# Performance work log

Measured on AMD Instinct MI355X. Metric: run time of the kernel, lower is better.

The kernel has to match this reference:

```python
import jax, jax.numpy as jnp
import numpy as np

N_NODES = 50000
N_EDGES = 400000
N_GRAPHS = 256
HID = 128
FEAT_IN, POS_IN, EDGE_IN = 64, 16, 16
N_LAYERS = 4


def _lin(x, w, b):
    return x @ w.T + b


def setup_inputs() -> dict:
    key = jax.random.key(0)
    ks = iter(jax.random.split(key, 64))
    s = 0.05

    def w(shape):
        return (jax.random.normal(next(ks), shape, dtype=jnp.float32) * s)

    inp = {
        "h": jax.random.normal(next(ks), (N_NODES, FEAT_IN), dtype=jnp.float32),
        "e": jax.random.normal(next(ks), (N_EDGES, EDGE_IN), dtype=jnp.float32),
        "p": jax.random.normal(next(ks), (N_NODES, POS_IN), dtype=jnp.float32),
        "edge_index": jax.random.randint(next(ks), (2, N_EDGES), 0, N_NODES),
        "batch": jnp.sort(jax.random.randint(next(ks), (N_NODES,), 0, N_GRAPHS)),
        # embeddings
        "h_embed_w": w((HID, FEAT_IN)), "h_embed_b": w((HID,)),
        "e_embed_w": w((HID, EDGE_IN)), "e_embed_b": w((HID,)),
        "p_embed_w": w((HID, POS_IN)), "p_embed_b": w((HID,)),
        # per-layer params, stacked over layers
        "hu_w": w((N_LAYERS, HID, 5 * HID)), "hu_b": w((N_LAYERS, HID)),
        "eu_w": w((N_LAYERS, HID, 3 * HID)), "eu_b": w((N_LAYERS, HID)),
        "pu_w": w((N_LAYERS, HID, 3 * HID)), "pu_b": w((N_LAYERS, HID)),
        "hagg_w": w((N_LAYERS, HID, 2 * HID)), "hagg_b": w((N_LAYERS, HID)),
        "pagg_w": w((N_LAYERS, HID, 2 * HID)), "pagg_b": w((N_LAYERS, HID)),
        # readout MLP
        "r1_w": w((HID, 2 * HID)), "r1_b": w((HID,)),
        "r2_w": w((HID // 2, HID)), "r2_b": w((HID // 2,)),
        "r3_w": w((1, HID // 2)), "r3_b": w((1,)),
    }
    return inp


def reference(h, e, p, edge_index, batch,
              h_embed_w, h_embed_b, e_embed_w, e_embed_b, p_embed_w, p_embed_b,
              hu_w, hu_b, eu_w, eu_b, pu_w, pu_b,
              hagg_w, hagg_b, pagg_w, pagg_b,
              r1_w, r1_b, r2_w, r2_b, r3_w, r3_b):
    send, rec = edge_index[0], edge_index[1]
    N = h.shape[0]

    h = _lin(h, h_embed_w, h_embed_b)
    e = _lin(e, e_embed_w, e_embed_b)
    p = _lin(p, p_embed_w, p_embed_b)

    for l in range(N_LAYERS):
        hp_send = jnp.concatenate((h[send], p[send]), axis=1)  # [E, 2H]
        hp_rec = jnp.concatenate((h[rec], p[rec]), axis=1)     # [E, 2H]
        h_msg = _lin(jnp.concatenate((hp_send, hp_rec, e), axis=1), hu_w[l], hu_b[l])
        h_msg_agg = jax.ops.segment_sum(h_msg, rec, num_segments=N)
        h = _lin(jnp.concatenate((h, h_msg_agg), axis=1), hagg_w[l], hagg_b[l])
        e = _lin(jnp.concatenate((h[send], h[rec], e), axis=1), eu_w[l], eu_b[l])
        p_msg = _lin(jnp.concatenate((p[send], p[rec], e), axis=1), pu_w[l], pu_b[l])
        p_msg_agg = jax.ops.segment_sum(p_msg, rec, num_segments=N)
        p = _lin(jnp.concatenate((p, p_msg_agg), axis=1), pagg_w[l], pagg_b[l])

    h_agg = jax.ops.segment_sum(h, batch, num_segments=N_GRAPHS)
    p_agg = jax.ops.segment_sum(p, batch, num_segments=N_GRAPHS)
    hep = jnp.concatenate((h_agg, p_agg), axis=1)
    x = jax.nn.relu(_lin(hep, r1_w, r1_b))
    x = jax.nn.relu(_lin(x, r2_w, r2_b))
    out = _lin(x, r3_w, r3_b).squeeze(-1)  # [N_GRAPHS]
    return (out, p)
```

## Files before the change

kernel.cpp:

```cpp
#include <hip/hip_runtime.h>

typedef __attribute__((ext_vector_type(8))) short bf16x8;
typedef __attribute__((ext_vector_type(4))) float f32x4;
typedef __attribute__((ext_vector_type(4))) unsigned short us4;

__device__ __forceinline__ float b2f(unsigned short h) {
  union { unsigned int u; float f; } v; v.u = ((unsigned int)h) << 16; return v.f;
}
__device__ __forceinline__ unsigned short f2b(float f) {
  union { float f; unsigned int u; } v; v.f = f;
  unsigned int r = v.u + 0x7fffu + ((v.u >> 16) & 1u);
  return (unsigned short)(r >> 16);
}

__global__ void f2b_kernel(const float* __restrict__ in, unsigned short* __restrict__ out, int n4) {
  int i = blockIdx.x * blockDim.x + threadIdx.x;
  int stride = gridDim.x * blockDim.x;
  for (; i < n4; i += stride) {
    float4 v = reinterpret_cast<const float4*>(in)[i];
    us4 o;
    o[0] = f2b(v.x); o[1] = f2b(v.y); o[2] = f2b(v.z); o[3] = f2b(v.w);
    reinterpret_cast<us4*>(out)[i] = o;
  }
}

__launch_bounds__(256)
__global__ void compose_w(const float* __restrict__ hg, const float* __restrict__ hu,
                          const float* __restrict__ pg, const float* __restrict__ pu,
                          const float* __restrict__ hub, const float* __restrict__ pub,
                          unsigned short* __restrict__ wh, unsigned short* __restrict__ wp,
                          float* __restrict__ bh, float* __restrict__ bp) {
  __shared__ float As[128][129];
  __shared__ float Bs[128][36];
  __shared__ float bvs[128];
  const int l = blockIdx.x >> 5, t = blockIdx.x & 31;
  const float* A; const float* B; const float* bv; unsigned short* W; float* bo;
  int lda, ldb, K2, ldw, cbase;
  if (t < 20) {
    A = hg + (size_t)l * 128 * 256; lda = 256;
    B = hu + (size_t)l * 128 * 640; ldb = 640; K2 = 640;
    W = wh + (size_t)l * 128 * 768; ldw = 768;
    bv = hub + l * 128; bo = bh + l * 128; cbase = t * 32;
  } else {
    A = pg + (size_t)l * 128 * 256; lda = 256;
    B = pu + (size_t)l * 128 * 384; ldb = 384; K2 = 384;
    W = wp + (size_t)l * 128 * 512; ldw = 512;
    bv = pub + l * 128; bo = bp + l * 128; cbase = (t - 20) * 32;
  }
  const int tid = threadIdx.x;
  for (int idx = tid; idx < 128 * 128; idx += 256) {
    int r = idx >> 7, c = idx & 127;
    As[r][c] = A[r * lda + 128 + c];
  }
  for (int idx = tid; idx < 128 * 32; idx += 256) {
    int m = idx >> 5, c = idx & 31;
    Bs[m][c] = B[m * ldb + cbase + c];
  }
  if (tid < 128) bvs[tid] = bv[tid];
  __syncthreads();
  const int o = tid & 127, g = tid >> 7;
  float acc[16];
#pragma unroll
  for (int j = 0; j < 16; ++j) acc[j] = 0.f;
  for (int m = 0; m < 128; ++m) {
    float a = As[o][m];
#pragma unroll
    for (int j4 = 0; j4 < 4; ++j4) {
      float4 b4 = *reinterpret_cast<const float4*>(&Bs[m][g * 16 + j4 * 4]);
      acc[j4 * 4 + 0] += a * b4.x; acc[j4 * 4 + 1] += a * b4.y;
      acc[j4 * 4 + 2] += a * b4.z; acc[j4 * 4 + 3] += a * b4.w;
    }
  }
#pragma unroll
  for (int j4 = 0; j4 < 4; ++j4) {
    us4 ov;
    ov[0] = f2b(acc[j4 * 4 + 0]); ov[1] = f2b(acc[j4 * 4 + 1]);
    ov[2] = f2b(acc[j4 * 4 + 2]); ov[3] = f2b(acc[j4 * 4 + 3]);
    *reinterpret_cast<us4*>(&W[(long)o * ldw + cbase + g * 16 + j4 * 4]) = ov;
  }
  if (cbase == 0) {
    for (int idx = tid; idx < 128 * 128; idx += 256) {
      int oo = idx >> 7, m = idx & 127;
      W[(long)oo * ldw + K2 + m] = f2b(A[oo * lda + m]);
    }
    if (tid < 128) {
      float s = 0.f;
      for (int m = 0; m < 128; ++m) s += As[tid][m] * bvs[m];
      bo[tid] = s;
    }
  }
}

template<int K>
__launch_bounds__(256)
__global__ void embed_fast(const float* __restrict__ in, const float* __restrict__ w,
                           const float* __restrict__ b, unsigned short* __restrict__ out,
                           long M, int ostride, int ocoloff, const float* __restrict__ degB,
                           unsigned short* __restrict__ out2, const float* __restrict__ scaleF) {
  __shared__ float wT[K][129];
  __shared__ float xt[16 * K];
  const int tid = threadIdx.x;
  const int col = tid & 127;
  const int half = tid >> 7;
  for (int idx = tid; idx < 128 * K; idx += 256) {
    int c = idx / K, k = idx % K;
    wT[k][c] = w[idx];
  }
  __syncthreads();
  float wreg[K];
#pragma unroll
  for (int k = 0; k < K; ++k) wreg[k] = wT[k][col];
  const float bcol = b[col];

  for (long r0 = (long)blockIdx.x * 16; r0 < M; r0 += (long)gridDim.x * 16) {
    __syncthreads();
    const float4* src4 = reinterpret_cast<const float4*>(in + r0 * K);
    const int n4 = 16 * K / 4;
    if (r0 + 16 <= M) {
      for (int i = tid; i < n4; i += 256)
        reinterpret_cast<float4*>(xt)[i] = src4[i];
    } else {
      int rem = (int)((M - r0) * K) / 4;
      for (int i = tid; i < n4; i += 256) {
        float4 z = {0.f, 0.f, 0.f, 0.f};
        reinterpret_cast<float4*>(xt)[i] = (i < rem) ? src4[i] : z;
      }
    }
    __syncthreads();
#pragma unroll
    for (int rr = 0; rr < 8; ++rr) {
      long row = r0 + half * 8 + rr;
      if (row >= M) break;
      const float* xr = &xt[(half * 8 + rr) * K];
      float acc = bcol * (degB ? degB[row] : 1.0f);
#pragma unroll
      for (int k4 = 0; k4 < K / 4; ++k4) {
        float4 xv = reinterpret_cast<const float4*>(xr)[k4];
        acc += xv.x * wreg[k4 * 4] + xv.y * wreg[k4 * 4 + 1] +
               xv.z * wreg[k4 * 4 + 2] + xv.w * wreg[k4 * 4 + 3];
      }
      long o = row * ostride + ocoloff + col;
      out[o] = f2b(acc);
      if (out2) out2[o] = f2b(acc * scaleF[row]);
    }
  }
}

__global__ void count_deg(const int* __restrict__ rec, int* __restrict__ deg, int E) {
  int i = blockIdx.x * blockDim.x + threadIdx.x;
  if (i < E) atomicAdd(&deg[rec[i]], 1);
}

__global__ void scan_blk(const int* __restrict__ deg, int* __restrict__ tmp,
                         int* __restrict__ blkSum, int N) {
  __shared__ int ts[256];
  const int b = blockIdx.x, t = threadIdx.x;
  const int base = b * 1024 + t * 4;
  int v0 = (base + 0 < N) ? deg[base + 0] : 0;
  int v1 = (base + 1 < N) ? deg[base + 1] : 0;
  int v2 = (base + 2 < N) ? deg[base + 2] : 0;
  int v3 = (base + 3 < N) ? deg[base + 3] : 0;
  int tsum = v0 + v1 + v2 + v3;
  ts[t] = tsum;
  __syncthreads();
  for (int off = 1; off < 256; off <<= 1) {
    int x = (t >= off) ? ts[t - off] : 0;
    __syncthreads();
    ts[t] += x;
    __syncthreads();
  }
  int texcl = ts[t] - tsum;
  if (base + 0 < N) tmp[base + 0] = texcl;
  if (base + 1 < N) tmp[base + 1] = texcl + v0;
  if (base + 2 < N) tmp[base + 2] = texcl + v0 + v1;
  if (base + 3 < N) tmp[base + 3] = texcl + v0 + v1 + v2;
  if (t == 255) blkSum[b] = ts[255];
}

__global__ void scan_top(int* __restrict__ blkSum, int nb) {
  __shared__ int s[64];
  int t = threadIdx.x;
  if (t < nb) s[t] = blkSum[t];
  __syncthreads();
  if (t == 0) {
    int run = 0;
    for (int i = 0; i < nb; ++i) { int x = s[i]; s[i] = run; run += x; }
  }
  __syncthreads();
  if (t < nb) blkSum[t] = s[t];
}

__global__ void scan_fix(const int* __restrict__ deg, int* __restrict__ row_ptr,
                         const int* __restrict__ blkOff, int* __restrict__ cursor,
                         float* __restrict__ degF, int N, int E) {
  const int b = blockIdx.x, t = threadIdx.x;
  const int base = b * 1024 + t * 4;
  const int off = blkOff[b];
#pragma unroll
  for (int k = 0; k < 4; ++k) {
    int i = base + k;
    if (i < N) {
      int v = row_ptr[i] + off;
      row_ptr[i] = v;
      cursor[i] = v;
      degF[i] = (float)deg[i];
    }
  }
  if (b == 0 && t == 0) row_ptr[N] = E;
}

__global__ void scatter_perm(const int* __restrict__ rec, const int* __restrict__ send,
                             int* __restrict__ cursor, int* __restrict__ perm,
                             int* __restrict__ sendP, int E) {
  int i = blockIdx.x * blockDim.x + threadIdx.x;
  if (i < E) {
    int pos = atomicAdd(&cursor[rec[i]], 1);
    perm[pos] = i;
    sendP[pos] = send[i];
  }
}

__global__ void segsum_raw(const float* __restrict__ eraw, const int* __restrict__ row_ptr,
                           const int* __restrict__ perm, float* __restrict__ out16, int N) {
  int sub = threadIdx.x >> 4;
  int f = threadIdx.x & 15;
  int r = blockIdx.x * 16 + sub;
  if (r >= N) return;
  int j0 = row_ptr[r], j1 = row_ptr[r + 1];
  float s0 = 0.f, s1 = 0.f;
  int j = j0;
  for (; j + 2 <= j1; j += 2) {
    int e0 = perm[j], e1 = perm[j + 1];
    s0 += eraw[(long)e0 * 16 + f];
    s1 += eraw[(long)e1 * 16 + f];
  }
  if (j < j1) s0 += eraw[(long)perm[j] * 16 + f];
  out16[(long)r * 16 + f] = s0 + s1;
}

__launch_bounds__(256)
__global__ void gather_sum256(const unsigned short* __restrict__ src,
                              const int* __restrict__ row_ptr, const int* __restrict__ sendP,
                              unsigned short* __restrict__ dst, int N) {
  const int wid = threadIdx.x >> 6, lane = threadIdx.x & 63;
  const int r = blockIdx.x * 4 + wid;
  if (r >= N) return;
  const int j0 = row_ptr[r], j1 = row_ptr[r + 1];
  const int off = lane * 4;
  float a0 = 0.f, a1 = 0.f, a2 = 0.f, a3 = 0.f;
  int j = j0;
  for (; j + 4 <= j1; j += 4) {
    int i0 = sendP[j], i1 = sendP[j + 1], i2 = sendP[j + 2], i3 = sendP[j + 3];
    us4 x = *reinterpret_cast<const us4*>(&src[(long)i0 * 256 + off]);
    us4 y = *reinterpret_cast<const us4*>(&src[(long)i1 * 256 + off]);
    us4 z = *reinterpret_cast<const us4*>(&src[(long)i2 * 256 + off]);
    us4 w = *reinterpret_cast<const us4*>(&src[(long)i3 * 256 + off]);
    a0 += b2f(x[0]) + b2f(y[0]) + b2f(z[0]) + b2f(w[0]);
    a1 += b2f(x[1]) + b2f(y[1]) + b2f(z[1]) + b2f(w[1]);
    a2 += b2f(x[2]) + b2f(y[2]) + b2f(z[2]) + b2f(w[2]);
    a3 += b2f(x[3]) + b2f(y[3]) + b2f(z[3]) + b2f(w[3]);
  }
  for (; j < j1; ++j) {
    us4 x = *reinterpret_cast<const us4*>(&src[(long)sendP[j] * 256 + off]);
    a0 += b2f(x[0]); a1 += b2f(x[1]); a2 += b2f(x[2]); a3 += b2f(x[3]);
  }
  us4 o;
  o[0] = f2b(a0); o[1] = f2b(a1); o[2] = f2b(a2); o[3] = f2b(a3);
  *reinterpret_cast<us4*>(&dst[(long)r * 256 + off]) = o;
}

__launch_bounds__(256)
__global__ void gather_sum128(const unsigned short* __restrict__ src, int col,
                              const int* __restrict__ row_ptr, const int* __restrict__ sendP,
                              unsigned short* __restrict__ dst, int N) {
  const int wid = threadIdx.x >> 6, lane = threadIdx.x & 63;
  const int r = blockIdx.x * 4 + wid;
  if (r >= N) return;
  const int j0 = row_ptr[r], j1 = row_ptr[r + 1];
  const int half = lane >> 5;
  const int c = lane & 31;
  const int off = col + c * 4;
  float a0 = 0.f, a1 = 0.f, a2 = 0.f, a3 = 0.f;
  float b0 = 0.f, b1 = 0.f, b2 = 0.f, b3 = 0.f;
  int j = j0 + half;
  for (; j + 6 < j1; j += 8) {
    int i0 = sendP[j], i1 = sendP[j + 2], i2 = sendP[j + 4], i3 = sendP[j + 6];
    us4 x = *reinterpret_cast<const us4*>(&src[(long)i0 * 256 + off]);
    us4 y = *reinterpret_cast<const us4*>(&src[(long)i1 * 256 + off]);
    us4 z = *reinterpret_cast<const us4*>(&src[(long)i2 * 256 + off]);
    us4 w = *reinterpret_cast<const us4*>(&src[(long)i3 * 256 + off]);
    a0 += b2f(x[0]) + b2f(z[0]); a1 += b2f(x[1]) + b2f(z[1]);
    a2 += b2f(x[2]) + b2f(z[2]); a3 += b2f(x[3]) + b2f(z[3]);
    b0 += b2f(y[0]) + b2f(w[0]); b1 += b2f(y[1]) + b2f(w[1]);
    b2 += b2f(y[2]) + b2f(w[2]); b3 += b2f(y[3]) + b2f(w[3]);
  }
  for (; j + 2 < j1; j += 4) {
    int i0 = sendP[j], i1 = sendP[j + 2];
    us4 x = *reinterpret_cast<const us4*>(&src[(long)i0 * 256 + off]);
    us4 y = *reinterpret_cast<const us4*>(&src[(long)i1 * 256 + off]);
    a0 += b2f(x[0]); a1 += b2f(x[1]); a2 += b2f(x[2]); a3 += b2f(x[3]);
    b0 += b2f(y[0]); b1 += b2f(y[1]); b2 += b2f(y[2]); b3 += b2f(y[3]);
  }
  if (j < j1) {
    us4 x = *reinterpret_cast<const us4*>(&src[(long)sendP[j] * 256 + off]);
    a0 += b2f(x[0]); a1 += b2f(x[1]); a2 += b2f(x[2]); a3 += b2f(x[3]);
  }
  a0 += b0; a1 += b1; a2 += b2; a3 += b3;
  a0 += __shfl_xor(a0, 32); a1 += __shfl_xor(a1, 32);
  a2 += __shfl_xor(a2, 32); a3 += __shfl_xor(a3, 32);
  if (half == 0) {
    us4 o;
    o[0] = f2b(a0); o[1] = f2b(a1); o[2] = f2b(a2); o[3] = f2b(a3);
    *reinterpret_cast<us4*>(&dst[(long)r * 256 + off]) = o;
  }
}

__launch_bounds__(256, 3)
__global__ void gemm_mp(int M, int nsrc, int strides, int coloffs,
                        const unsigned short* __restrict__ sp0, const unsigned short* __restrict__ sp1,
                        const unsigned short* __restrict__ sp2, const unsigned short* __restrict__ sp3,
                        const unsigned short* __restrict__ sp4, const unsigned short* __restrict__ sp5,
                        const unsigned short* __restrict__ Wb,
                        const float* __restrict__ bdeg, const float* __restrict__ bone,
                        const float* __restrict__ degF,
                        unsigned short* __restrict__ outB, int ostride, int ocoloff,
                        unsigned short* __restrict__ outB2, float* __restrict__ outF) {
  __shared__ __align__(16) unsigned short ldsW[8 * 64 * 8];
  const int tid = threadIdx.x;
  const int wid = tid >> 6, lane = tid & 63;
  const int K = nsrc * 128;
  const long rowBase = (long)blockIdx.x * 128 + wid * 32;
  const int lq = lane >> 4;
  const int lr = lane & 15;

  int rowD[2];
#pragma unroll
  for (int am = 0; am < 2; ++am) {
    long e = rowBase + am * 16 + lr;
    if (e >= M) e = M - 1;
    rowD[am] = (int)e;
  }

  f32x4 acc[2][8];
#pragma unroll
  for (int i = 0; i < 2; ++i)
#pragma unroll
    for (int j = 0; j < 8; ++j) acc[i][j] = 0.f;

  for (int si = 0; si < nsrc; ++si) {
    const unsigned short* sp = (si == 0) ? sp0 : (si == 1) ? sp1 : (si == 2) ? sp2
                              : (si == 3) ? sp3 : (si == 4) ? sp4 : sp5;
    const long astride = (long)(((strides >> (si * 4)) & 15) * 128);
    const int acoloff = ((coloffs >> (si * 4)) & 15) * 128;
#pragma unroll
    for (int sub = 0; sub < 4; ++sub) {
      const int koff = acoloff + sub * 32 + lq * 8;
      bf16x8 a[2];
#pragma unroll
      for (int am = 0; am < 2; ++am)
        a[am] = *reinterpret_cast<const bf16x8*>(&sp[(long)rowD[am] * astride + koff]);
      __syncthreads();
#pragma unroll
      for (int it = 0; it < 2; ++it) {
        int idx = tid + it * 256;
        int t = idx >> 6, l = idx & 63;
        int n = t * 16 + (l & 15);
        int kk = si * 128 + sub * 32 + ((l >> 4) * 8);
        *reinterpret_cast<bf16x8*>(&ldsW[idx * 8]) =
            *reinterpret_cast<const bf16x8*>(&Wb[(long)n * K + kk]);
      }
      __syncthreads();
#pragma unroll
      for (int n = 0; n < 8; ++n) {
        bf16x8 b = *reinterpret_cast<const bf16x8*>(&ldsW[(n * 64 + lane) * 8]);
#pragma unroll
        for (int am = 0; am < 2; ++am)
          acc[am][n] = __builtin_amdgcn_mfma_f32_16x16x32_bf16(a[am], b, acc[am][n], 0, 0, 0);
      }
    }
  }

  float bd[8], bo[8];
#pragma unroll
  for (int n = 0; n < 8; ++n) {
    bd[n] = bdeg ? bdeg[n * 16 + lr] : 0.f;
    bo[n] = bone ? bone[n * 16 + lr] : 0.f;
  }

#pragma unroll
  for (int am = 0; am < 2; ++am) {
#pragma unroll
    for (int r = 0; r < 4; ++r) {
      long row = rowBase + am * 16 + lq * 4 + r;
      if (row < M) {
        float d = degF[row];
        long ob = row * ostride + ocoloff;
#pragma unroll
        for (int n = 0; n < 8; ++n) {
          float v = acc[am][n][r] + bd[n] * d + bo[n];
          outB[ob + n * 16 + lr] = f2b(v);
          if (outB2) outB2[ob + n * 16 + lr] = f2b(v * d);
          if (outF) outF[row * 128 + n * 16 + lr] = v;
        }
      }
    }
  }
}

__global__ void readout_agg(const unsigned short* __restrict__ hp,
                            const int* __restrict__ batch, float* __restrict__ hep, int N) {
  int col = threadIdx.x;
  int n0 = blockIdx.x * 128;
  int n1 = n0 + 128; if (n1 > N) n1 = N;
  float sum = 0.f; int curg = -1;
  for (int n = n0; n < n1; ++n) {
    int g = batch[n];
    if (g != curg) {
      if (curg >= 0) unsafeAtomicAdd(&hep[(long)curg * 256 + col], sum);
      curg = g; sum = 0.f;
    }
    sum += b2f(hp[(long)n * 256 + col]);
  }
  if (curg >= 0) unsafeAtomicAdd(&hep[(long)curg * 256 + col], sum);
}

__global__ void mlp_kernel(const float* __restrict__ hep,
                           const float* __restrict__ r1w, const float* __restrict__ r1b,
                           const float* __restrict__ r2w, const float* __restrict__ r2b,
                           const float* __restrict__ r3w, const float* __restrict__ r3b,
                           float* __restrict__ out) {
  int g = blockIdx.x, t = threadIdx.x;
  __shared__ float x[256];
  __shared__ float y[128];
  __shared__ float z[64];
  x[t] = hep[(long)g * 256 + t];
  x[t + 128] = hep[(long)g * 256 + 128 + t];
  __syncthreads();
  float s = r1b[t];
  for (int k = 0; k < 256; ++k) s += r1w[t * 256 + k] * x[k];
  y[t] = fmaxf(s, 0.f);
  __syncthreads();
  if (t < 64) {
    float s2 = r2b[t];
    for (int k = 0; k < 128; ++k) s2 += r2w[t * 128 + k] * y[k];
    z[t] = fmaxf(s2, 0.f);
  }
  __syncthreads();
  if (t == 0) {
    float s3 = r3b[0];
    for (int k = 0; k < 64; ++k) s3 += r3w[k] * z[k];
    out[g] = s3;
  }
}

extern "C" void kernel_launch(void* const* d_in, const int* in_sizes, int n_in,
                              void* d_out, int out_size, void* d_ws, size_t ws_size,
                              hipStream_t stream) {
  const float* h_in = (const float*)d_in[0];
  const float* e_in = (const float*)d_in[1];
  const float* p_in = (const float*)d_in[2];
  const int* ei = (const int*)d_in[3];
  const int* batch = (const int*)d_in[4];
  const float* he_w = (const float*)d_in[5];  const float* he_b = (const float*)d_in[6];
  const float* ee_w = (const float*)d_in[7];  const float* ee_b = (const float*)d_in[8];
  const float* pe_w = (const float*)d_in[9];  const float* pe_b = (const float*)d_in[10];
  const float* hu_w = (const float*)d_in[11]; const float* hu_b = (const float*)d_in[12];
  const float* eu_w = (const float*)d_in[13]; const float* eu_b = (const float*)d_in[14];
  const float* pu_w = (const float*)d_in[15]; const float* pu_b = (const float*)d_in[16];
  const float* hg_w = (const float*)d_in[17]; const float* hg_b = (const float*)d_in[18];
  const float* pg_w = (const float*)d_in[19]; const float* pg_b = (const float*)d_in[20];
  const float* r1w = (const float*)d_in[21];  const float* r1b = (const float*)d_in[22];
  const float* r2w = (const float*)d_in[23];  const float* r2b = (const float*)d_in[24];
  const float* r3w = (const float*)d_in[25];  const float* r3b = (const float*)d_in[26];

  const int N = 50000, E = 400000, G = 256;
  const int* send = ei;
  const int* rec = ei + E;

  char* ws = (char*)d_ws;
  size_t off = 0;
  auto alloc = [&](size_t bytes) {
    void* pp = ws + off;
    off += (bytes + 255) & ~(size_t)255;
    return pp;
  };
  unsigned short* hp  = (unsigned short*)alloc((size_t)N * 256 * 2);
  unsigned short* dhp = (unsigned short*)alloc((size_t)N * 256 * 2);
  unsigned short* gHP = (unsigned short*)alloc((size_t)N * 256 * 2);
  unsigned short* sT  = (unsigned short*)alloc((size_t)N * 128 * 2);
  float* segsumF = (float*)alloc((size_t)N * 16 * 4);
  int* deg = (int*)alloc((size_t)N * 4);
  int* row_ptr = (int*)alloc((size_t)(N + 1) * 4);
  int* cursor = (int*)alloc((size_t)N * 4);
  int* blkSum = (int*)alloc((size_t)64 * 4);
  int* perm = (int*)alloc((size_t)E * 4);
  int* sendP = (int*)alloc((size_t)E * 4);
  float* degF = (float*)alloc((size_t)N * 4);
  float* hep = (float*)alloc((size_t)G * 256 * 4);
  unsigned short* w_h2 = (unsigned short*)alloc((size_t)4 * 128 * 768 * 2);
  unsigned short* w_p2 = (unsigned short*)alloc((size_t)4 * 128 * 512 * 2);
  unsigned short* w_eu = (unsigned short*)alloc((size_t)4 * 128 * 384 * 2);
  float* bh1 = (float*)alloc((size_t)4 * 128 * 4);
  float* bp1 = (float*)alloc((size_t)4 * 128 * 4);
  (void)ws_size; (void)n_in; (void)in_sizes; (void)out_size;

  f2b_kernel<<<192, 256, 0, stream>>>(eu_w, w_eu, 4 * 128 * 384 / 4);
  compose_w<<<128, 256, 0, stream>>>(hg_w, hu_w, pg_w, pu_w, hu_b, pu_b, w_h2, w_p2, bh1, bp1);

  const int nb = (N + 1023) / 1024;
  hipMemsetAsync(deg, 0, (size_t)N * 4, stream);
  count_deg<<<(E + 255) / 256, 256, 0, stream>>>(rec, deg, E);
  scan_blk<<<nb, 256, 0, stream>>>(deg, row_ptr, blkSum, N);
  scan_top<<<1, 64, 0, stream>>>(blkSum, nb);
  scan_fix<<<nb, 256, 0, stream>>>(deg, row_ptr, blkSum, cursor, degF, N, E);
  scatter_perm<<<(E + 255) / 256, 256, 0, stream>>>(rec, send, cursor, perm, sendP, E);

  embed_fast<64><<<3125, 256, 0, stream>>>(h_in, he_w, he_b, hp, N, 256, 0, nullptr, dhp, degF);
  embed_fast<16><<<3125, 256, 0, stream>>>(p_in, pe_w, pe_b, hp, N, 256, 128, nullptr, dhp, degF);
  segsum_raw<<<(N + 15) / 16, 256, 0, stream>>>(e_in, row_ptr, perm, segsumF, N);
  embed_fast<16><<<3125, 256, 0, stream>>>(segsumF, ee_w, ee_b, sT, N, 128, 0, degF, nullptr, nullptr);

  gather_sum256<<<(N + 3) / 4, 256, 0, stream>>>(hp, row_ptr, sendP, gHP, N);

  float* pOut = (float*)d_out + 256;
  const int gridN = (N + 127) / 128;
  const int gridG = (N + 3) / 4;

  for (int l = 0; l < 4; ++l) {
    gemm_mp<<<gridN, 256, 0, stream>>>(N, 6, 0x212222, 0x001010,
        gHP, gHP, dhp, dhp, sT, hp,
        w_h2 + (size_t)l * 128 * 768, bh1 + l * 128, hg_b + l * 128, degF,
        hp, 256, 0, dhp, nullptr);
    gather_sum128<<<gridG, 256, 0, stream>>>(hp, 0, row_ptr, sendP, gHP, N);
    gemm_mp<<<gridN, 256, 0, stream>>>(N, 3, 0x122, 0x000,
        gHP, dhp, sT, nullptr, nullptr, nullptr,
        w_eu + (size_t)l * 128 * 384, eu_b + l * 128, nullptr, degF,
        sT, 128, 0, nullptr, nullptr);
    gemm_mp<<<gridN, 256, 0, stream>>>(N, 4, 0x2122, 0x1011,
        gHP, dhp, sT, hp, nullptr, nullptr,
        w_p2 + (size_t)l * 128 * 512, bp1 + l * 128, pg_b + l * 128, degF,
        hp, 256, 128, (l < 3) ? dhp : nullptr, (l == 3) ? pOut : nullptr);
    if (l < 3)
      gather_sum128<<<gridG, 256, 0, stream>>>(hp, 128, row_ptr, sendP, gHP, N);
  }

  hipMemsetAsync(hep, 0, (size_t)G * 256 * 4, stream);
  readout_agg<<<(N + 127) / 128, 256, 0, stream>>>(hp, batch, hep, N);
  mlp_kernel<<<G, 128, 0, stream>>>(hep, r1w, r1b, r2w, r2b, r3w, r3b, (float*)d_out);
}
```

Before: 700.1 us.

## Drop degree-scaled dhp buffer; scale A fragments by degree inside GEMM

Removes the separately materialized degree-scaled copy (dhp) of node features. The GEMM now reuses each loaded A tile twice, once raw and once multiplied in-register by the node degree, and the composed weight columns are reordered to match. This cuts global writes of the scaled buffer in the embed and GEMM epilogues and halves A-side reads for those sources. In exchange it adds per-element bf16 scaling ALU work and an extra LDS weight-staging round with syncs per repeated source.

```diff
diff --git a/kernel.cpp b/kernel.cpp
--- a/kernel.cpp
+++ b/kernel.cpp
@@ -11,6 +11,18 @@
   union { float f; unsigned int u; } v; v.f = f;
   unsigned int r = v.u + 0x7fffu + ((v.u >> 16) & 1u);
   return (unsigned short)(r >> 16);
+}
+
+__device__ __forceinline__ bf16x8 scale8(bf16x8 a, float d) {
+  bf16x8 r;
+#pragma unroll
+  for (int i = 0; i < 8; ++i) {
+    union { unsigned int u; float f; } v;
+    v.u = ((unsigned int)(unsigned short)a[i]) << 16;
+    v.f *= d;
+    r[i] = (short)(v.u >> 16);
+  }
+  return r;
 }
 
 __global__ void f2b_kernel(const float* __restrict__ in, unsigned short* __restrict__ out, int n4) {
@@ -35,17 +47,21 @@
   __shared__ float bvs[128];
   const int l = blockIdx.x >> 5, t = blockIdx.x & 31;
   const float* A; const float* B; const float* bv; unsigned short* W; float* bo;
-  int lda, ldb, K2, ldw, cbase;
+  int lda, ldb, ldw, cbase, wbase, dbase;
   if (t < 20) {
     A = hg + (size_t)l * 128 * 256; lda = 256;
-    B = hu + (size_t)l * 128 * 640; ldb = 640; K2 = 640;
+    B = hu + (size_t)l * 128 * 640; ldb = 640;
     W = wh + (size_t)l * 128 * 768; ldw = 768;
     bv = hub + l * 128; bo = bh + l * 128; cbase = t * 32;
+    wbase = (cbase < 256) ? cbase : (cbase < 512 ? cbase + 256 : cbase - 256);
+    dbase = 384;
   } else {
     A = pg + (size_t)l * 128 * 256; lda = 256;
-    B = pu + (size_t)l * 128 * 384; ldb = 384; K2 = 384;
+    B = pu + (size_t)l * 128 * 384; ldb = 384;
     W = wp + (size_t)l * 128 * 512; ldw = 512;
     bv = pub + l * 128; bo = bp + l * 128; cbase = (t - 20) * 32;
+    wbase = (cbase < 128) ? cbase : (cbase < 256 ? cbase + 256 : cbase - 128);
+    dbase = 256;
   }
   const int tid = threadIdx.x;
   for (int idx = tid; idx < 128 * 128; idx += 256) {
@@ -76,12 +92,12 @@
     us4 ov;
     ov[0] = f2b(acc[j4 * 4 + 0]); ov[1] = f2b(acc[j4 * 4 + 1]);
     ov[2] = f2b(acc[j4 * 4 + 2]); ov[3] = f2b(acc[j4 * 4 + 3]);
-    *reinterpret_cast<us4*>(&W[(long)o * ldw + cbase + g * 16 + j4 * 4]) = ov;
+    *reinterpret_cast<us4*>(&W[(long)o * ldw + wbase + g * 16 + j4 * 4]) = ov;
   }
   if (cbase == 0) {
     for (int idx = tid; idx < 128 * 128; idx += 256) {
       int oo = idx >> 7, m = idx & 127;
-      W[(long)oo * ldw + K2 + m] = f2b(A[oo * lda + m]);
+      W[(long)oo * ldw + dbase + m] = f2b(A[oo * lda + m]);
     }
     if (tid < 128) {
       float s = 0.f;
@@ -95,8 +111,7 @@
 __launch_bounds__(256)
 __global__ void embed_fast(const float* __restrict__ in, const float* __restrict__ w,
                            const float* __restrict__ b, unsigned short* __restrict__ out,
-                           long M, int ostride, int ocoloff, const float* __restrict__ degB,
-                           unsigned short* __restrict__ out2, const float* __restrict__ scaleF) {
+                           long M, int ostride, int ocoloff, const float* __restrict__ degB) {
   __shared__ float wT[K][129];
   __shared__ float xt[16 * K];
   const int tid = threadIdx.x;
@@ -139,9 +154,7 @@
         acc += xv.x * wreg[k4 * 4] + xv.y * wreg[k4 * 4 + 1] +
                xv.z * wreg[k4 * 4 + 2] + xv.w * wreg[k4 * 4 + 3];
       }
-      long o = row * ostride + ocoloff + col;
-      out[o] = f2b(acc);
-      if (out2) out2[o] = f2b(acc * scaleF[row]);
+      out[row * ostride + ocoloff + col] = f2b(acc);
     }
   }
 }
@@ -316,29 +329,29 @@
 }
 
 __launch_bounds__(256, 3)
-__global__ void gemm_mp(int M, int nsrc, int strides, int coloffs,
+__global__ void gemm_mp(int M, int nsrc, int Kw, int srcsel, int coloffs, int sflags,
                         const unsigned short* __restrict__ sp0, const unsigned short* __restrict__ sp1,
-                        const unsigned short* __restrict__ sp2, const unsigned short* __restrict__ sp3,
-                        const unsigned short* __restrict__ sp4, const unsigned short* __restrict__ sp5,
+                        const unsigned short* __restrict__ sp2,
                         const unsigned short* __restrict__ Wb,
                         const float* __restrict__ bdeg, const float* __restrict__ bone,
                         const float* __restrict__ degF,
                         unsigned short* __restrict__ outB, int ostride, int ocoloff,
-                        unsigned short* __restrict__ outB2, float* __restrict__ outF) {
+                        float* __restrict__ outF) {
   __shared__ __align__(16) unsigned short ldsW[8 * 64 * 8];
   const int tid = threadIdx.x;
   const int wid = tid >> 6, lane = tid & 63;
-  const int K = nsrc * 128;
   const long rowBase = (long)blockIdx.x * 128 + wid * 32;
   const int lq = lane >> 4;
   const int lr = lane & 15;
 
   int rowD[2];
+  float degD[2];
 #pragma unroll
   for (int am = 0; am < 2; ++am) {
     long e = rowBase + am * 16 + lr;
     if (e >= M) e = M - 1;
     rowD[am] = (int)e;
+    degD[am] = degF[rowD[am]];
   }
 
   f32x4 acc[2][8];
@@ -347,37 +360,46 @@
 #pragma unroll
     for (int j = 0; j < 8; ++j) acc[i][j] = 0.f;
 
+  int wcol = 0;
   for (int si = 0; si < nsrc; ++si) {
-    const unsigned short* sp = (si == 0) ? sp0 : (si == 1) ? sp1 : (si == 2) ? sp2
-                              : (si == 3) ? sp3 : (si == 4) ? sp4 : sp5;
-    const long astride = (long)(((strides >> (si * 4)) & 15) * 128);
+    const int sel = (srcsel >> (si * 4)) & 15;
+    const unsigned short* sp = (sel == 0) ? sp0 : (sel == 1) ? sp1 : sp2;
+    const long astride = (sel == 2) ? 128 : 256;
     const int acoloff = ((coloffs >> (si * 4)) & 15) * 128;
-#pragma unroll
+    const int f = (sflags >> (si * 4)) & 15;
+    const int nrep = (f == 1) ? 2 : 1;
+#pragma unroll 4
     for (int sub = 0; sub < 4; ++sub) {
       const int koff = acoloff + sub * 32 + lq * 8;
       bf16x8 a[2];
 #pragma unroll
       for (int am = 0; am < 2; ++am)
         a[am] = *reinterpret_cast<const bf16x8*>(&sp[(long)rowD[am] * astride + koff]);
-      __syncthreads();
-#pragma unroll
-      for (int it = 0; it < 2; ++it) {
-        int idx = tid + it * 256;
-        int t = idx >> 6, l = idx & 63;
-        int n = t * 16 + (l & 15);
-        int kk = si * 128 + sub * 32 + ((l >> 4) * 8);
-        *reinterpret_cast<bf16x8*>(&ldsW[idx * 8]) =
-            *reinterpret_cast<const bf16x8*>(&Wb[(long)n * K + kk]);
+      for (int rep = 0; rep < nrep; ++rep) {
+        const bool sc = (f == 2) || (rep == 1);
+        const int wk = wcol + rep * 128 + sub * 32;
+        __syncthreads();
+#pragma unroll
+        for (int it = 0; it < 2; ++it) {
+          int idx = tid + it * 256;
+          int t = idx >> 6, l = idx & 63;
+          int n = t * 16 + (l & 15);
+          int kk = wk + ((l >> 4) * 8);
+          *reinterpret_cast<bf16x8*>(&ldsW[idx * 8]) =
+              *reinterpret_cast<const bf16x8*>(&Wb[(long)n * Kw + kk]);
+        }
+        __syncthreads();
+        bf16x8 av0 = sc ? scale8(a[0], degD[0]) : a[0];
+        bf16x8 av1 = sc ? scale8(a[1], degD[1]) : a[1];
+#pragma unroll
+        for (int n = 0; n < 8; ++n) {
+          bf16x8 b = *reinterpret_cast<const bf16x8*>(&ldsW[(n * 64 + lane) * 8]);
+          acc[0][n] = __builtin_amdgcn_mfma_f32_16x16x32_bf16(av0, b, acc[0][n], 0, 0, 0);
+          acc[1][n] = __builtin_amdgcn_mfma_f32_16x16x32_bf16(av1, b, acc[1][n], 0, 0, 0);
+        }
       }
-      __syncthreads();
-#pragma unroll
-      for (int n = 0; n < 8; ++n) {
-        bf16x8 b = *reinterpret_cast<const bf16x8*>(&ldsW[(n * 64 + lane) * 8]);
-#pragma unroll
-        for (int am = 0; am < 2; ++am)
-          acc[am][n] = __builtin_amdgcn_mfma_f32_16x16x32_bf16(a[am], b, acc[am][n], 0, 0, 0);
-      }
-    }
+    }
+    wcol += nrep * 128;
   }
 
   float bd[8], bo[8];
@@ -399,7 +421,6 @@
         for (int n = 0; n < 8; ++n) {
           float v = acc[am][n][r] + bd[n] * d + bo[n];
           outB[ob + n * 16 + lr] = f2b(v);
-          if (outB2) outB2[ob + n * 16 + lr] = f2b(v * d);
           if (outF) outF[row * 128 + n * 16 + lr] = v;
         }
       }
@@ -485,7 +506,6 @@
     return pp;
   };
   unsigned short* hp  = (unsigned short*)alloc((size_t)N * 256 * 2);
-  unsigned short* dhp = (unsigned short*)alloc((size_t)N * 256 * 2);
   unsigned short* gHP = (unsigned short*)alloc((size_t)N * 256 * 2);
   unsigned short* sT  = (unsigned short*)alloc((size_t)N * 128 * 2);
   float* segsumF = (float*)alloc((size_t)N * 16 * 4);
@@ -515,10 +535,10 @@
   scan_fix<<<nb, 256, 0, stream>>>(deg, row_ptr, blkSum, cursor, degF, N, E);
   scatter_perm<<<(E + 255) / 256, 256, 0, stream>>>(rec, send, cursor, perm, sendP, E);
 
-  embed_fast<64><<<3125, 256, 0, stream>>>(h_in, he_w, he_b, hp, N, 256, 0, nullptr, dhp, degF);
-  embed_fast<16><<<3125, 256, 0, stream>>>(p_in, pe_w, pe_b, hp, N, 256, 128, nullptr, dhp, degF);
+  embed_fast<64><<<3125, 256, 0, stream>>>(h_in, he_w, he_b, hp, N, 256, 0, nullptr);
+  embed_fast<16><<<3125, 256, 0, stream>>>(p_in, pe_w, pe_b, hp, N, 256, 128, nullptr);
   segsum_raw<<<(N + 15) / 16, 256, 0, stream>>>(e_in, row_ptr, perm, segsumF, N);
-  embed_fast<16><<<3125, 256, 0, stream>>>(segsumF, ee_w, ee_b, sT, N, 128, 0, degF, nullptr, nullptr);
+  embed_fast<16><<<3125, 256, 0, stream>>>(segsumF, ee_w, ee_b, sT, N, 128, 0, degF);
 
   gather_sum256<<<(N + 3) / 4, 256, 0, stream>>>(hp, row_ptr, sendP, gHP, N);
 
@@ -527,19 +547,19 @@
   const int gridG = (N + 3) / 4;
 
   for (int l = 0; l < 4; ++l) {
-    gemm_mp<<<gridN, 256, 0, stream>>>(N, 6, 0x212222, 0x001010,
-        gHP, gHP, dhp, dhp, sT, hp,
+    gemm_mp<<<gridN, 256, 0, stream>>>(N, 5, 768, 0x11200, 0x10010, 0x21000,
+        gHP, hp, sT,
         w_h2 + (size_t)l * 128 * 768, bh1 + l * 128, hg_b + l * 128, degF,
-        hp, 256, 0, dhp, nullptr);
+        hp, 256, 0, nullptr);
     gather_sum128<<<gridG, 256, 0, stream>>>(hp, 0, row_ptr, sendP, gHP, N);
-    gemm_mp<<<gridN, 256, 0, stream>>>(N, 3, 0x122, 0x000,
-        gHP, dhp, sT, nullptr, nullptr, nullptr,
+    gemm_mp<<<gridN, 256, 0, stream>>>(N, 3, 384, 0x210, 0x000, 0x020,
+        gHP, hp, sT,
         w_eu + (size_t)l * 128 * 384, eu_b + l * 128, nullptr, degF,
-        sT, 128, 0, nullptr, nullptr);
-    gemm_mp<<<gridN, 256, 0, stream>>>(N, 4, 0x2122, 0x1011,
-        gHP, dhp, sT, hp, nullptr, nullptr,
+        sT, 128, 0, nullptr);
+    gemm_mp<<<gridN, 256, 0, stream>>>(N, 3, 512, 0x120, 0x101, 0x100,
+        gHP, hp, sT,
         w_p2 + (size_t)l * 128 * 512, bp1 + l * 128, pg_b + l * 128, degF,
-        hp, 256, 128, (l < 3) ? dhp : nullptr, (l == 3) ? pOut : nullptr);
+        hp, 256, 128, (l == 3) ? pOut : nullptr);
     if (l < 3)
       gather_sum128<<<gridG, 256, 0, stream>>>(hp, 128, row_ptr, sendP, gHP, N);
   }
```

After: 658.7 us. 1.06x faster.
